# Optimization experiments

Measured on AMD Instinct MI355X. Metric: run time of the kernel, lower is better.

The kernel has to match this reference:

```python
import jax, jax.numpy as jnp
import numpy as np

B, T, D = 4, 4096, 768      # batch, tokens, n_embd
S = 1024                    # memory_slots (divides T -> adaptive pool == window mean)
K = 8                       # memory_topk
RW = 0.1                    # memory_retrieval_weight


def setup_inputs() -> dict:
    key = jax.random.key(0)
    ks = jax.random.split(key, 10)
    w = 1.0 / np.sqrt(D).astype(np.float32)
    return {
        "x": jax.random.normal(ks[0], (B, T, D), jnp.float32),
        "Wq": jax.random.normal(ks[1], (D, D), jnp.float32) * w,
        "bq": jnp.zeros((D,), jnp.float32),
        "Wk": jax.random.normal(ks[2], (D, D), jnp.float32) * w,
        "bk": jnp.zeros((D,), jnp.float32),
        "Wv": jax.random.normal(ks[3], (D, D), jnp.float32) * w,
        "bv": jnp.zeros((D,), jnp.float32),
        "Wp": jax.random.normal(ks[4], (D, D), jnp.float32) * w,
        "bp": jnp.zeros((D,), jnp.float32),
        "persistent_memory": jax.random.normal(ks[5], (S, D), jnp.float32),
    }


def reference(x, Wq, bq, Wk, bk, Wv, bv, Wp, bp, persistent_memory):
    # _build_memory_slots: adaptive_avg_pool1d to S slots; T % S == 0 so it is a window mean
    pooled = x.reshape(B, S, T // S, D).mean(axis=2)                    # [B,S,D]
    pers = jnp.broadcast_to(persistent_memory[None], (B, S, D))         # persistent bank
    slots = jnp.concatenate([pooled, pers], axis=1)                     # [B,2S,D]

    q = x @ Wq + bq                                                     # [B,T,D]
    k = slots @ Wk + bk                                                 # [B,2S,D]
    v = slots @ Wv + bv                                                 # [B,2S,D]

    scores = jnp.einsum('btd,bsd->bts', q, k) / jnp.sqrt(jnp.float32(D))  # [B,T,2S]
    top_s, top_i = jax.lax.top_k(scores, K)                             # [B,T,K]
    w = jax.nn.softmax(top_s, axis=-1)                                  # softmax over top-k only

    # gather top-k values: [B,T,K,D]
    vg = jnp.take_along_axis(v, top_i.reshape(B, T * K)[:, :, None], axis=1)
    vg = vg.reshape(B, T, K, D)
    retrieved = jnp.einsum('btk,btkd->btd', w, vg)                      # weighted combine

    return RW * (retrieved @ Wp + bp)                                   # proj * retrieval_weight
```

## Files before the change

kernel.cpp:

```cpp
#include <hip/hip_runtime.h>
#include <math.h>

#define BB 4
#define TT 4096
#define DD 768
#define SS 1024
#define S2 2048
#define KTOP 8
#define RWEIGHT 0.1f
#define TAU 2e-4f
#define AMB_CAP 256

typedef __attribute__((ext_vector_type(8))) _Float16 f16x8;
typedef __attribute__((ext_vector_type(4))) float f32x4;
typedef _Float16 f16;

__global__ __launch_bounds__(256) void build_pooled_all(
    const float* __restrict__ x, float* __restrict__ slots)
{
    int i = blockIdx.x * 256 + threadIdx.x;
    int s2 = i / DD;
    int d = i - s2 * DD;
    int b = s2 >> 10, s = s2 & 1023;
    const float* xb = x + (size_t)b * TT * DD + (size_t)(4 * s) * DD + d;
    slots[i] = 0.25f * (xb[0] + xb[DD] + xb[2 * DD] + xb[3 * DD]);
}

__global__ __launch_bounds__(256) void transpose_split(
    const float* __restrict__ W0, const float* __restrict__ W1,
    const float* __restrict__ W2, const float* __restrict__ W3,
    f16* __restrict__ WQh, f16* __restrict__ WQm,
    f16* __restrict__ WKh, f16* __restrict__ WKm,
    f16* __restrict__ WVh, f16* __restrict__ WPh,
    float* __restrict__ WkT32)
{
    const int z = blockIdx.z;
    const float* W = (z == 0) ? W0 : (z == 1) ? W1 : (z == 2) ? W2 : W3;
    __shared__ float t[32][33];
    int bx = blockIdx.x * 32, by = blockIdx.y * 32;
    int lx = threadIdx.x & 31, ly = threadIdx.x >> 5;
#pragma unroll
    for (int r = 0; r < 32; r += 8)
        t[ly + r][lx] = W[(size_t)(bx + ly + r) * 768 + by + lx];
    __syncthreads();
#pragma unroll
    for (int r = 0; r < 32; r += 8) {
        float w = t[lx][ly + r];
        size_t idx = (size_t)(by + ly + r) * 768 + bx + lx;
        f16 h = (f16)w;
        if (z == 0) { WQh[idx] = h; WQm[idx] = (f16)(w - (float)h); }
        else if (z == 1) { WKh[idx] = h; WKm[idx] = (f16)(w - (float)h); WkT32[idx] = w; }
        else if (z == 2) { WVh[idx] = h; }
        else { WPh[idx] = h; }
    }
}

__global__ void zeroN(int* p) { p[threadIdx.x] = 0; }

__device__ __forceinline__ void tile_split_prod(
    const float* __restrict__ A, int arow0,
    const f16* __restrict__ Bh, const f16* __restrict__ Bm, int bncol,
    const float* __restrict__ bias,
    f16* __restrict__ Ch, f16* __restrict__ Cm, int crow0,
    f16* LAh, f16* LAm, f16* LBh, f16* LBm)
{
    const int tid = threadIdx.x;
    const int lane = tid & 63;
    const int wc = (tid >> 6) & 1;
    const int wr = (tid >> 7) & 1;
    const int srow = tid >> 1, c0 = tid & 1;
    const int p0 = c0 ^ (srow & 3) ^ ((srow >> 2) & 1);
    const int wo0 = srow * 32 + p0 * 8, wo1 = wo0 ^ 16;
    const int csw = (((lane >> 4) ^ (lane & 3) ^ ((lane >> 2) & 1)) * 8);
    const size_t bn = (size_t)bncol;

    f32x4 acc[4][4];
#pragma unroll
    for (int i = 0; i < 4; ++i)
#pragma unroll
        for (int j = 0; j < 4; ++j) acc[i][j] = (f32x4){0.f, 0.f, 0.f, 0.f};

    const float* pa = A + (size_t)(arow0 + srow) * 768 + c0 * 8;
    const f16* pbh = Bh + (bn + srow) * 768 + c0 * 8;
    const f16* pbm = Bm + (bn + srow) * 768 + c0 * 8;

    for (int k0 = 0; k0 < 768; k0 += 32) {
        float4 a0 = *(const float4*)(pa + k0);
        float4 a1 = *(const float4*)(pa + k0 + 4);
        float4 a2 = *(const float4*)(pa + k0 + 16);
        float4 a3 = *(const float4*)(pa + k0 + 20);
        f16x8 bh0 = *(const f16x8*)(pbh + k0);
        f16x8 bh1 = *(const f16x8*)(pbh + k0 + 16);
        f16x8 bm0 = *(const f16x8*)(pbm + k0);
        f16x8 bm1 = *(const f16x8*)(pbm + k0 + 16);
        __syncthreads();
        {
            float av[16] = {a0.x, a0.y, a0.z, a0.w, a1.x, a1.y, a1.z, a1.w,
                            a2.x, a2.y, a2.z, a2.w, a3.x, a3.y, a3.z, a3.w};
            f16x8 h, m;
#pragma unroll
            for (int j = 0; j < 8; ++j) {
                f16 hh = (f16)av[j]; h[j] = hh; m[j] = (f16)(av[j] - (float)hh);
            }
            *(f16x8*)&LAh[wo0] = h; *(f16x8*)&LAm[wo0] = m;
#pragma unroll
            for (int j = 0; j < 8; ++j) {
                f16 hh = (f16)av[j + 8]; h[j] = hh; m[j] = (f16)(av[j + 8] - (float)hh);
            }
            *(f16x8*)&LAh[wo1] = h; *(f16x8*)&LAm[wo1] = m;
            *(f16x8*)&LBh[wo0] = bh0; *(f16x8*)&LBh[wo1] = bh1;
            *(f16x8*)&LBm[wo0] = bm0; *(f16x8*)&LBm[wo1] = bm1;
        }
        __syncthreads();

        f16x8 fah[4], fam[4], fbh[4], fbm[4];
#pragma unroll
        for (int mi = 0; mi < 4; ++mi) {
            int off = (wr * 64 + mi * 16 + (lane & 15)) * 32 + csw;
            fah[mi] = *(const f16x8*)&LAh[off];
            fam[mi] = *(const f16x8*)&LAm[off];
        }
#pragma unroll
        for (int ni = 0; ni < 4; ++ni) {
            int off = (wc * 64 + ni * 16 + (lane & 15)) * 32 + csw;
            fbh[ni] = *(const f16x8*)&LBh[off];
            fbm[ni] = *(const f16x8*)&LBm[off];
        }
#pragma unroll
        for (int mi = 0; mi < 4; ++mi)
#pragma unroll
            for (int ni = 0; ni < 4; ++ni) {
                acc[mi][ni] = __builtin_amdgcn_mfma_f32_16x16x32_f16(
                    fah[mi], fbh[ni], acc[mi][ni], 0, 0, 0);
                acc[mi][ni] = __builtin_amdgcn_mfma_f32_16x16x32_f16(
                    fah[mi], fbm[ni], acc[mi][ni], 0, 0, 0);
                acc[mi][ni] = __builtin_amdgcn_mfma_f32_16x16x32_f16(
                    fam[mi], fbh[ni], acc[mi][ni], 0, 0, 0);
            }
    }

    const int orow0 = wr * 64 + (lane >> 4) * 4;
    const int ocol0 = wc * 64 + (lane & 15);
#pragma unroll
    for (int mi = 0; mi < 4; ++mi)
#pragma unroll
        for (int ni = 0; ni < 4; ++ni) {
            size_t col = bn + ocol0 + ni * 16;
            float badd = bias[col];
            size_t rbase = (size_t)crow0 + orow0 + mi * 16;
#pragma unroll
            for (int r = 0; r < 4; ++r) {
                float val = acc[mi][ni][r] + badd;
                f16 h = (f16)val;
                size_t idx = (rbase + r) * 768 + col;
                Ch[idx] = h;
                Cm[idx] = (f16)(val - (float)h);
            }
        }
}

__device__ __forceinline__ void tile_1p_prod(
    const float* __restrict__ A, int arow0,
    const f16* __restrict__ Bh, int bncol,
    const float* __restrict__ bias,
    f16* __restrict__ Co, int crow0, f16* LA, f16* LB)
{
    const int tid = threadIdx.x;
    const int lane = tid & 63;
    const int wc = (tid >> 6) & 1;
    const int wr = (tid >> 7) & 1;
    const int srow = tid >> 1, c0 = tid & 1;
    const int p0 = c0 ^ (srow & 3) ^ ((srow >> 2) & 1);
    const int wo0 = srow * 32 + p0 * 8, wo1 = wo0 ^ 16;
    const int csw = (((lane >> 4) ^ (lane & 3) ^ ((lane >> 2) & 1)) * 8);
    const size_t bn = (size_t)bncol;

    f32x4 acc[4][4];
#pragma unroll
    for (int i = 0; i < 4; ++i)
#pragma unroll
        for (int j = 0; j < 4; ++j) acc[i][j] = (f32x4){0.f, 0.f, 0.f, 0.f};

    const float* pa = A + (size_t)(arow0 + srow) * 768 + c0 * 8;
    const f16* pbh = Bh + (bn + srow) * 768 + c0 * 8;

    for (int k0 = 0; k0 < 768; k0 += 32) {
        float4 a0 = *(const float4*)(pa + k0);
        float4 a1 = *(const float4*)(pa + k0 + 4);
        float4 a2 = *(const float4*)(pa + k0 + 16);
        float4 a3 = *(const float4*)(pa + k0 + 20);
        f16x8 bh0 = *(const f16x8*)(pbh + k0);
        f16x8 bh1 = *(const f16x8*)(pbh + k0 + 16);
        __syncthreads();
        {
            f16x8 h;
            h[0] = (f16)a0.x; h[1] = (f16)a0.y; h[2] = (f16)a0.z; h[3] = (f16)a0.w;
            h[4] = (f16)a1.x; h[5] = (f16)a1.y; h[6] = (f16)a1.z; h[7] = (f16)a1.w;
            *(f16x8*)&LA[wo0] = h;
            h[0] = (f16)a2.x; h[1] = (f16)a2.y; h[2] = (f16)a2.z; h[3] = (f16)a2.w;
            h[4] = (f16)a3.x; h[5] = (f16)a3.y; h[6] = (f16)a3.z; h[7] = (f16)a3.w;
            *(f16x8*)&LA[wo1] = h;
            *(f16x8*)&LB[wo0] = bh0;
            *(f16x8*)&LB[wo1] = bh1;
        }
        __syncthreads();
        f16x8 fah[4], fbh[4];
#pragma unroll
        for (int mi = 0; mi < 4; ++mi)
            fah[mi] = *(const f16x8*)&LA[(wr * 64 + mi * 16 + (lane & 15)) * 32 + csw];
#pragma unroll
        for (int ni = 0; ni < 4; ++ni)
            fbh[ni] = *(const f16x8*)&LB[(wc * 64 + ni * 16 + (lane & 15)) * 32 + csw];
#pragma unroll
        for (int mi = 0; mi < 4; ++mi)
#pragma unroll
            for (int ni = 0; ni < 4; ++ni)
                acc[mi][ni] = __builtin_amdgcn_mfma_f32_16x16x32_f16(
                    fah[mi], fbh[ni], acc[mi][ni], 0, 0, 0);
    }

    const int orow0 = wr * 64 + (lane >> 4) * 4;
    const int ocol0 = wc * 64 + (lane & 15);
#pragma unroll
    for (int mi = 0; mi < 4; ++mi)
#pragma unroll
        for (int ni = 0; ni < 4; ++ni) {
            size_t col = bn + ocol0 + ni * 16;
            float badd = bias[col];
            size_t rbase = (size_t)crow0 + orow0 + mi * 16;
#pragma unroll
            for (int r = 0; r < 4; ++r)
                Co[(rbase + r) * 768 + col] = (f16)(acc[mi][ni][r] + badd);
        }
}

__device__ __forceinline__ void tile_proj(
    const f16* __restrict__ A, int arow0,
    const f16* __restrict__ Bh, int bncol,
    const float* __restrict__ bias,
    float* __restrict__ Co, int crow0, f16* LA, f16* LB)
{
    const int tid = threadIdx.x;
    const int lane = tid & 63;
    const int wc = (tid >> 6) & 1;
    const int wr = (tid >> 7) & 1;
    const int srow = tid >> 1, c0 = tid & 1;
    const int p0 = c0 ^ (srow & 3) ^ ((srow >> 2) & 1);
    const int wo0 = srow * 32 + p0 * 8, wo1 = wo0 ^ 16;
    const int csw = (((lane >> 4) ^ (lane & 3) ^ ((lane >> 2) & 1)) * 8);
    const size_t bn = (size_t)bncol;

    f32x4 acc[4][4];
#pragma unroll
    for (int i = 0; i < 4; ++i)
#pragma unroll
        for (int j = 0; j < 4; ++j) acc[i][j] = (f32x4){0.f, 0.f, 0.f, 0.f};

    const f16* pa = A + (size_t)(arow0 + srow) * 768 + c0 * 8;
    const f16* pbh = Bh + (bn + srow) * 768 + c0 * 8;

    for (int k0 = 0; k0 < 768; k0 += 32) {
        f16x8 ah0 = *(const f16x8*)(pa + k0);
        f16x8 ah1 = *(const f16x8*)(pa + k0 + 16);
        f16x8 bh0 = *(const f16x8*)(pbh + k0);
        f16x8 bh1 = *(const f16x8*)(pbh + k0 + 16);
        __syncthreads();
        *(f16x8*)&LA[wo0] = ah0; *(f16x8*)&LA[wo1] = ah1;
        *(f16x8*)&LB[wo0] = bh0; *(f16x8*)&LB[wo1] = bh1;
        __syncthreads();
        f16x8 fah[4], fbh[4];
#pragma unroll
        for (int mi = 0; mi < 4; ++mi)
            fah[mi] = *(const f16x8*)&LA[(wr * 64 + mi * 16 + (lane & 15)) * 32 + csw];
#pragma unroll
        for (int ni = 0; ni < 4; ++ni)
            fbh[ni] = *(const f16x8*)&LB[(wc * 64 + ni * 16 + (lane & 15)) * 32 + csw];
#pragma unroll
        for (int mi = 0; mi < 4; ++mi)
#pragma unroll
            for (int ni = 0; ni < 4; ++ni)
                acc[mi][ni] = __builtin_amdgcn_mfma_f32_16x16x32_f16(
                    fah[mi], fbh[ni], acc[mi][ni], 0, 0, 0);
    }

    const int orow0 = wr * 64 + (lane >> 4) * 4;
    const int ocol0 = wc * 64 + (lane & 15);
#pragma unroll
    for (int mi = 0; mi < 4; ++mi)
#pragma unroll
        for (int ni = 0; ni < 4; ++ni) {
            size_t col = bn + ocol0 + ni * 16;
            float badd = RWEIGHT * bias[col];
            size_t rbase = (size_t)crow0 + orow0 + mi * 16;
#pragma unroll
            for (int r = 0; r < 4; ++r)
                Co[(rbase + r) * 768 + col] = RWEIGHT * acc[mi][ni][r] + badd;
        }
}

__device__ __forceinline__ void tile_scores_planes(
    const f16* __restrict__ qh, const f16* __restrict__ qm, int arow0,
    const f16* __restrict__ kh, const f16* __restrict__ km, int bncol,
    float* __restrict__ C, float alpha,
    f16* LAh, f16* LAm, f16* LBh, f16* LBm)
{
    const int tid = threadIdx.x;
    const int lane = tid & 63;
    const int wc = (tid >> 6) & 1;
    const int wr = (tid >> 7) & 1;
    const int srow = tid >> 1, c0 = tid & 1;
    const int p0 = c0 ^ (srow & 3) ^ ((srow >> 2) & 1);
    const int wo0 = srow * 32 + p0 * 8, wo1 = wo0 ^ 16;
    const int csw = (((lane >> 4) ^ (lane & 3) ^ ((lane >> 2) & 1)) * 8);
    const size_t bn = (size_t)bncol;

    f32x4 acc[4][4];
#pragma unroll
    for (int i = 0; i < 4; ++i)
#pragma unroll
        for (int j = 0; j < 4; ++j) acc[i][j] = (f32x4){0.f, 0.f, 0.f, 0.f};

    const f16* pah = qh + (size_t)(arow0 + srow) * 768 + c0 * 8;
    const f16* pam = qm + (size_t)(arow0 + srow) * 768 + c0 * 8;
    const f16* pbh = kh + (bn + srow) * 768 + c0 * 8;
    const f16* pbm = km + (bn + srow) * 768 + c0 * 8;

    for (int k0 = 0; k0 < 768; k0 += 32) {
        f16x8 ah0 = *(const f16x8*)(pah + k0);
        f16x8 ah1 = *(const f16x8*)(pah + k0 + 16);
        f16x8 am0 = *(const f16x8*)(pam + k0);
        f16x8 am1 = *(const f16x8*)(pam + k0 + 16);
        f16x8 bh0 = *(const f16x8*)(pbh + k0);
        f16x8 bh1 = *(const f16x8*)(pbh + k0 + 16);
        f16x8 bm0 = *(const f16x8*)(pbm + k0);
        f16x8 bm1 = *(const f16x8*)(pbm + k0 + 16);
        __syncthreads();
        *(f16x8*)&LAh[wo0] = ah0; *(f16x8*)&LAh[wo1] = ah1;
        *(f16x8*)&LAm[wo0] = am0; *(f16x8*)&LAm[wo1] = am1;
        *(f16x8*)&LBh[wo0] = bh0; *(f16x8*)&LBh[wo1] = bh1;
        *(f16x8*)&LBm[wo0] = bm0; *(f16x8*)&LBm[wo1] = bm1;
        __syncthreads();

        f16x8 fah[4], fam[4], fbh[4], fbm[4];
#pragma unroll
        for (int mi = 0; mi < 4; ++mi) {
            int off = (wr * 64 + mi * 16 + (lane & 15)) * 32 + csw;
            fah[mi] = *(const f16x8*)&LAh[off];
            fam[mi] = *(const f16x8*)&LAm[off];
        }
#pragma unroll
        for (int ni = 0; ni < 4; ++ni) {
            int off = (wc * 64 + ni * 16 + (lane & 15)) * 32 + csw;
            fbh[ni] = *(const f16x8*)&LBh[off];
            fbm[ni] = *(const f16x8*)&LBm[off];
        }
#pragma unroll
        for (int mi = 0; mi < 4; ++mi)
#pragma unroll
            for (int ni = 0; ni < 4; ++ni) {
                acc[mi][ni] = __builtin_amdgcn_mfma_f32_16x16x32_f16(
                    fah[mi], fbh[ni], acc[mi][ni], 0, 0, 0);
                acc[mi][ni] = __builtin_amdgcn_mfma_f32_16x16x32_f16(
                    fah[mi], fbm[ni], acc[mi][ni], 0, 0, 0);
                acc[mi][ni] = __builtin_amdgcn_mfma_f32_16x16x32_f16(
                    fam[mi], fbh[ni], acc[mi][ni], 0, 0, 0);
            }
    }

    const int orow0 = wr * 64 + (lane >> 4) * 4;
    const int ocol0 = wc * 64 + (lane & 15);
#pragma unroll
    for (int mi = 0; mi < 4; ++mi)
#pragma unroll
        for (int ni = 0; ni < 4; ++ni) {
            size_t col = bn + ocol0 + ni * 16;
            size_t rbase = (size_t)arow0 + orow0 + mi * 16;
#pragma unroll
            for (int r = 0; r < 4; ++r)
                C[(rbase + r) * S2 + col] = alpha * acc[mi][ni][r];
        }
}

__global__ __launch_bounds__(256) void megaSelProd(
    int nSel, const float* __restrict__ scores, const f16* __restrict__ v16r,
    f16* __restrict__ retrW, int gbase,
    int* __restrict__ ambc, int* __restrict__ ambgrow, int* __restrict__ cand,
    float* __restrict__ oldw, f16* __restrict__ vsave,
    int hasQ, int hasKV, int doPm,
    const float* __restrict__ xq, const float* __restrict__ slots_b,
    const float* __restrict__ pm,
    const f16* __restrict__ WQh, const f16* __restrict__ WQm,
    const f16* __restrict__ WKh, const f16* __restrict__ WKm,
    const f16* __restrict__ WVh,
    const float* __restrict__ bq, const float* __restrict__ bk,
    const float* __restrict__ bv,
    f16* __restrict__ qh, f16* __restrict__ qm,
    f16* __restrict__ kh, f16* __restrict__ km,
    f16* __restrict__ v16w, f16* __restrict__ v16w2)
{
    __shared__ f16 LAh[4096], LAm[4096], LBh[4096], LBm[4096];
    int t = blockIdx.x;

    if (hasQ) {
        if (t < 192) {
            tile_split_prod(xq, (t / 6) * 128, WQh, WQm, (t % 6) * 128, bq,
                            qh, qm, (t / 6) * 128, LAh, LAm, LBh, LBm);
            return;
        }
        t -= 192;
    }
    if (hasKV) {
        if (t < 48) {
            tile_split_prod(slots_b, (t / 6) * 128, WKh, WKm, (t % 6) * 128, bk,
                            kh, km, (t / 6) * 128, LAh, LAm, LBh, LBm);
            return;
        }
        t -= 48;
        if (doPm) {
            if (t < 48) {
                tile_split_prod(pm, (t / 6) * 128, WKh, WKm, (t % 6) * 128, bk,
                                kh, km, 1024 + (t / 6) * 128, LAh, LAm, LBh, LBm);
                return;
            }
            t -= 48;
        }
        if (t < 48) {
            tile_1p_prod(slots_b, (t / 6) * 128, WVh, (t % 6) * 128, bv,
                         v16w, (t / 6) * 128, LAh, LBh);
            return;
        }
        t -= 48;
        if (doPm) {
            if (t < 48) {
                tile_1p_prod(pm, (t / 6) * 128, WVh, (t % 6) * 128, bv,
                             v16w, 1024 + (t / 6) * 128, LAh, LBh);
                return;
            }
            t -= 48;
            if (t < 48) {
                tile_1p_prod(pm, (t / 6) * 128, WVh, (t % 6) * 128, bv,
                             v16w2, 1024 + (t / 6) * 128, LAh, LBh);
                return;
            }
            t -= 48;
        }
    }
    if (t >= nSel) return;

    const int lane = threadIdx.x & 63;
    const int wave = threadIdx.x >> 6;
    const int row = t * 4 + wave;
    const float* srow = scores + (size_t)row * S2;
    float vals[32];
#pragma unroll
    for (int i = 0; i < 32; ++i) vals[i] = srow[lane + (i << 6)];

    float topv[16]; int topi[16];
    bool amb = false;
    int nr = 9;
    for (int r = 0; r < 16; ++r) {
        if (r >= nr) break;
        float bvv = -3.4e38f; int bii = 0x7fffffff;
#pragma unroll
        for (int i = 0; i < 32; ++i)
            if (vals[i] > bvv) { bvv = vals[i]; bii = lane + (i << 6); }
#pragma unroll
        for (int off = 32; off > 0; off >>= 1) {
            float ov = __shfl_xor(bvv, off);
            int   oi = __shfl_xor(bii, off);
            if (ov > bvv || (ov == bvv && oi < bii)) { bvv = ov; bii = oi; }
        }
        topv[r] = bvv; topi[r] = bii;
        if ((bii & 63) == lane) vals[bii >> 6] = -3.4e38f;
        if (r == 8) {
            amb = (topv[7] - topv[8]) < TAU;
            if (amb) nr = 16;
        }
    }

    float m = topv[0], w[KTOP], sum = 0.f;
#pragma unroll
    for (int r = 0; r < KTOP; ++r) { w[r] = expf(topv[r] - m); sum += w[r]; }
    float inv = 1.f / sum;
#pragma unroll
    for (int r = 0; r < KTOP; ++r) w[r] *= inv;

    if (amb) {
        int idx = 0;
        if (lane == 0) idx = atomicAdd(ambc, 1);
        idx = __shfl(idx, 0);
        if (idx < AMB_CAP) {
            if (lane == 0) ambgrow[idx] = gbase + row;
            if (lane < 16) cand[idx * 16 + lane] = topi[lane];
            if (lane < KTOP) oldw[idx * KTOP + lane] = w[lane];
            f16* vs = vsave + (size_t)idx * 16 * 768;
            for (int cc = lane; cc < 16 * 96; cc += 64) {
                int cr = cc / 96, ch = cc - cr * 96;
                *(f16x8*)&vs[(size_t)cr * 768 + ch * 8] =
                    *(const f16x8*)&v16r[(size_t)topi[cr] * 768 + ch * 8];
            }
        }
    }

    for (int c = lane; c < 96; c += 64) {
        float o[8] = {0, 0, 0, 0, 0, 0, 0, 0};
#pragma unroll
        for (int r = 0; r < KTOP; ++r) {
            f16x8 vv = *(const f16x8*)&v16r[(size_t)topi[r] * 768 + c * 8];
#pragma unroll
            for (int j = 0; j < 8; ++j) o[j] += w[r] * (float)vv[j];
        }
        f16x8 hx;
#pragma unroll
        for (int j = 0; j < 8; ++j) hx[j] = (f16)o[j];
        *(f16x8*)&retrW[(size_t)row * 768 + c * 8] = hx;
    }
}

__global__ __launch_bounds__(256) void megaScoresProj(
    int nSc, const f16* __restrict__ qh, const f16* __restrict__ qm,
    const f16* __restrict__ kh, const f16* __restrict__ km,
    float* __restrict__ scores, float alpha,
    const f16* __restrict__ retrR, const f16* __restrict__ WPh,
    const float* __restrict__ bp, float* __restrict__ outp)
{
    __shared__ f16 LAh[4096], LAm[4096], LBh[4096], LBm[4096];
    int t = blockIdx.x;
    if (t < nSc) {
        tile_scores_planes(qh, qm, (t >> 4) * 128, kh, km, (t & 15) * 128,
                           scores, alpha, LAh, LAm, LBh, LBm);
        return;
    }
    t -= nSc;
    tile_proj(retrR, (t / 6) * 128, WPh, (t % 6) * 128, bp,
              outp, (t / 6) * 128, LAh, LBh);
}

__global__ __launch_bounds__(256) void fixA(
    const int* __restrict__ amb_count, const int* __restrict__ amb_grow,
    const float* __restrict__ x, const float* __restrict__ Wq,
    const float* __restrict__ bq, double* __restrict__ q64buf)
{
    int n = *amb_count; if (n > AMB_CAP) n = AMB_CAP;
    const int i = blockIdx.y;
    if (i >= n) return;
    const int tid = threadIdx.x;
    const int jl = tid & 63;
    const int ks = tid >> 6;
    const int j = blockIdx.x * 64 + jl;
    const int grow = amb_grow[i];

    __shared__ float xs[768];
    __shared__ double ps[4][64];
    for (int t = tid; t < 768; t += 256) xs[t] = x[(size_t)grow * 768 + t];
    __syncthreads();

    double a0 = 0.0, a1 = 0.0;
    const float* wp = Wq + j;
    const int k0 = ks * 192;
#pragma unroll 8
    for (int k = 0; k < 192; k += 2) {
        a0 = fma((double)xs[k0 + k],     (double)wp[(size_t)(k0 + k) * 768],     a0);
        a1 = fma((double)xs[k0 + k + 1], (double)wp[(size_t)(k0 + k + 1) * 768], a1);
    }
    ps[ks][jl] = a0 + a1;
    __syncthreads();
    if (ks == 0)
        q64buf[(size_t)i * 768 + j] =
            ((ps[0][jl] + ps[1][jl]) + (ps[2][jl] + ps[3][jl])) + (double)bq[j];
}

__global__ __launch_bounds__(256) void fixB(
    const int* __restrict__ amb_count,
    const float* __restrict__ WkT, const float* __restrict__ bk,
    const double* __restrict__ q64buf,
    double* __restrict__ ubuf, double* __restrict__ bkqbuf)
{
    int n = *amb_count; if (n > AMB_CAP) n = AMB_CAP;
    const int i = blockIdx.y;
    if (i >= n) return;
    const int tid = threadIdx.x;
    const int tl = tid & 63;
    const int js = tid >> 6;
    const int t = blockIdx.x * 64 + tl;

    __shared__ double qs[768];
    __shared__ double ps[4][64];
    const double* qrow = q64buf + (size_t)i * 768;
    for (int k = tid; k < 768; k += 256) qs[k] = qrow[k];
    __syncthreads();

    double a0 = 0.0, a1 = 0.0;
    const float* wp = WkT + t;
    const int j0 = js * 192;
#pragma unroll 8
    for (int k = 0; k < 192; k += 2) {
        a0 = fma((double)wp[(size_t)(j0 + k) * 768],     qs[j0 + k],     a0);
        a1 = fma((double)wp[(size_t)(j0 + k + 1) * 768], qs[j0 + k + 1], a1);
    }
    ps[js][tl] = a0 + a1;
    __syncthreads();
    if (js == 0)
        ubuf[(size_t)i * 768 + t] = (ps[0][tl] + ps[1][tl]) + (ps[2][tl] + ps[3][tl]);

    if (blockIdx.x == 0 && tid < 64) {
        double p = 0.0;
#pragma unroll
        for (int c = 0; c < 12; ++c) {
            int jj = tid + (c << 6);
            p = fma((double)bk[jj], qs[jj], p);
        }
#pragma unroll
        for (int off = 32; off; off >>= 1) p += __shfl_xor(p, off);
        if (tid == 0) bkqbuf[i] = p;
    }
}

__global__ __launch_bounds__(256) void fixC(
    const int* __restrict__ amb_count, const int* __restrict__ amb_grow,
    const float* __restrict__ x, const float* __restrict__ pm,
    const int* __restrict__ cand, const float* __restrict__ oldw,
    const double* __restrict__ ubuf, const double* __restrict__ bkqbuf,
    const f16* __restrict__ vsave, float* __restrict__ dret)
{
    int n = *amb_count; if (n > AMB_CAP) n = AMB_CAP;
    const int i = blockIdx.x;
    if (i >= n) return;
    const int tid = threadIdx.x;
    const int lane = tid & 63;
    const int wave = tid >> 6;
    const int grow = amb_grow[i];
    const float* xb = x + (size_t)(grow >> 12) * TT * 768;

    __shared__ double us[768];
    __shared__ double cs_s[16];
    __shared__ float coef[16];

    const double* urow = ubuf + (size_t)i * 768;
    for (int t = tid; t < 768; t += 256) us[t] = urow[t];
    __syncthreads();

    const double ISQ = 1.0 / sqrt((double)DD);
    const double bkq = bkqbuf[i];
#pragma unroll
    for (int c = wave; c < 16; c += 4) {
        int s = cand[i * 16 + c];
        double p = 0.0;
        if (s < SS) {
            const float* xr = xb + (size_t)(4 * s) * 768;
#pragma unroll
            for (int t = 0; t < 12; ++t) {
                int j2 = lane + (t << 6);
                double sv = 0.25 * ((double)xr[j2] + (double)xr[j2 + 768] +
                                    (double)xr[j2 + 1536] + (double)xr[j2 + 2304]);
                p = fma(sv, us[j2], p);
            }
        } else {
            const float* pr = pm + (size_t)(s - SS) * 768;
#pragma unroll
            for (int t = 0; t < 12; ++t) {
                int j2 = lane + (t << 6);
                p = fma((double)pr[j2], us[j2], p);
            }
        }
#pragma unroll
        for (int off = 32; off; off >>= 1) p += __shfl_xor(p, off);
        if (lane == 0) cs_s[c] = (p + bkq) * ISQ;
    }
    __syncthreads();

    if (tid == 0) {
        double cs[16]; int ci[16];
        for (int c = 0; c < 16; ++c) { cs[c] = cs_s[c]; ci[c] = cand[i * 16 + c]; }
        unsigned used = 0;
        double sv[KTOP]; int sp[KTOP];
        for (int r = 0; r < KTOP; ++r) {
            int bi = -1;
            for (int c = 0; c < 16; ++c) {
                if (used & (1u << c)) continue;
                if (bi < 0 || cs[c] > cs[bi] ||
                    (cs[c] == cs[bi] && ci[c] < ci[bi])) bi = c;
            }
            used |= (1u << bi); sv[r] = cs[bi]; sp[r] = bi;
        }
        double mx = sv[0], es[KTOP], ssum = 0.0;
        for (int r = 0; r < KTOP; ++r) { es[r] = exp(sv[r] - mx); ssum += es[r]; }
        for (int c = 0; c < 16; ++c) coef[c] = (c < KTOP) ? -oldw[i * KTOP + c] : 0.f;
        for (int r = 0; r < KTOP; ++r) coef[sp[r]] += (float)(es[r] / ssum);
    }
    __syncthreads();

    const f16* vs = vsave + (size_t)i * 16 * 768;
    for (int j = tid; j < 768; j += 256) {
        float d = 0.f;
#pragma unroll
        for (int c = 0; c < 16; ++c) d += coef[c] * (float)vs[(size_t)c * 768 + j];
        dret[(size_t)i * 768 + j] = d;
    }
}

__global__ __launch_bounds__(256) void fixD(
    const int* __restrict__ amb_count, const int* __restrict__ amb_grow,
    const float* __restrict__ dret, const float* __restrict__ Wp,
    float* __restrict__ out)
{
    int n = *amb_count; if (n > AMB_CAP) n = AMB_CAP;
    const int i = blockIdx.y;
    if (i >= n) return;
    const int tid = threadIdx.x;
    const int jl = tid & 63;
    const int ks = tid >> 6;
    const int j = blockIdx.x * 64 + jl;
    const int grow = amb_grow[i];

    __shared__ float ds[768];
    __shared__ float ps[4][64];
    for (int t = tid; t < 768; t += 256) ds[t] = dret[(size_t)i * 768 + t];
    __syncthreads();

    float a0 = 0.f, a1 = 0.f;
    const float* wp = Wp + j;
    const int k0 = ks * 192;
#pragma unroll 8
    for (int k = 0; k < 192; k += 2) {
        a0 = fmaf(ds[k0 + k],     wp[(size_t)(k0 + k) * 768],     a0);
        a1 = fmaf(ds[k0 + k + 1], wp[(size_t)(k0 + k + 1) * 768], a1);
    }
    ps[ks][jl] = a0 + a1;
    __syncthreads();
    if (ks == 0)
        out[(size_t)grow * 768 + j] +=
            RWEIGHT * ((ps[0][jl] + ps[1][jl]) + (ps[2][jl] + ps[3][jl]));
}

extern "C" void kernel_launch(void* const* d_in, const int* in_sizes, int n_in,
                              void* d_out, int out_size, void* d_ws, size_t ws_size,
                              hipStream_t stream)
{
    const float* x  = (const float*)d_in[0];
    const float* Wq = (const float*)d_in[1];
    const float* bq = (const float*)d_in[2];
    const float* Wk = (const float*)d_in[3];
    const float* bk = (const float*)d_in[4];
    const float* Wv = (const float*)d_in[5];
    const float* bv = (const float*)d_in[6];
    const float* Wp = (const float*)d_in[7];
    const float* bp = (const float*)d_in[8];
    const float* pm = (const float*)d_in[9];
    float* out = (float*)d_out;
    float* ws  = (float*)d_ws;

    const float inv_sqrt_d = (float)(1.0 / sqrt((double)DD));
    const size_t TD  = (size_t)TT * DD;
    const size_t SD  = (size_t)SS * DD;
    const size_t WSZ = (size_t)DD * DD;

    float* p = ws;
    f16* WQh = (f16*)p; p += WSZ / 2;
    f16* WQm = (f16*)p; p += WSZ / 2;
    f16* WKh = (f16*)p; p += WSZ / 2;
    f16* WKm = (f16*)p; p += WSZ / 2;
    f16* WVh = (f16*)p; p += WSZ / 2;
    f16* WPh = (f16*)p; p += WSZ / 2;
    float* WkT32 = p; p += WSZ;
    float* slots_all = p; p += (size_t)BB * SD;
    f16* qh = (f16*)p; p += TD / 2;
    f16* qm = (f16*)p; p += TD / 2;
    f16* kh = (f16*)p; p += SD;
    f16* km = (f16*)p; p += SD;
    f16* v16a = (f16*)p; p += SD;
    f16* v16b = (f16*)p; p += SD;
    f16* retrA = (f16*)p; p += TD / 2;
    f16* retrB = (f16*)p; p += TD / 2;
    double* q64buf = (double*)p; p += (size_t)AMB_CAP * DD * 2;
    double* ubuf   = (double*)p; p += (size_t)AMB_CAP * DD * 2;
    double* bkqbuf = (double*)p; p += AMB_CAP * 2;
    int* cand = (int*)p; p += (size_t)AMB_CAP * 16;
    float* oldw = p; p += (size_t)AMB_CAP * KTOP;
    f16* vsave = (f16*)p; p += (size_t)AMB_CAP * 16 * DD / 2;
    float* dret = p; p += (size_t)AMB_CAP * DD;
    int* ambc = (int*)p; p += 64;
    int* ambgrow = (int*)p; p += AMB_CAP;
    float* scores = p;

    transpose_split<<<dim3(24, 24, 4), 256, 0, stream>>>(
        Wq, Wk, Wv, Wp, WQh, WQm, WKh, WKm, WVh, WPh, WkT32);
    zeroN<<<1, 64, 0, stream>>>(ambc);
    build_pooled_all<<<(BB * SS * DD) / 256, 256, 0, stream>>>(x, slots_all);

    megaSelProd<<<432, 256, 0, stream>>>(
        0, nullptr, nullptr, nullptr, 0, ambc, ambgrow, cand, oldw, vsave,
        1, 1, 1, x, slots_all, pm,
        WQh, WQm, WKh, WKm, WVh, bq, bk, bv, qh, qm, kh, km, v16a, v16b);
    megaScoresProj<<<512, 256, 0, stream>>>(
        512, qh, qm, kh, km, scores, inv_sqrt_d, nullptr, WPh, bp, nullptr);

    for (int b = 1; b < BB; ++b) {
        f16* v16w = (b & 1) ? v16b : v16a;
        f16* v16r = ((b - 1) & 1) ? v16b : v16a;
        f16* retrW = ((b - 1) & 1) ? retrB : retrA;

        megaSelProd<<<1312, 256, 0, stream>>>(
            1024, scores, v16r, retrW, (b - 1) * TT,
            ambc, ambgrow, cand, oldw, vsave,
            1, 1, 0, x + (size_t)b * TD, slots_all + (size_t)b * SD, nullptr,
            WQh, WQm, WKh, WKm, WVh, bq, bk, bv, qh, qm, kh, km, v16w, nullptr);
        megaScoresProj<<<704, 256, 0, stream>>>(
            512, qh, qm, kh, km, scores, inv_sqrt_d,
            retrW, WPh, bp, out + (size_t)(b - 1) * TD);
    }

    f16* v16r3 = v16b;
    f16* retrW3 = retrB;
    megaSelProd<<<1024, 256, 0, stream>>>(
        1024, scores, v16r3, retrW3, 3 * TT,
        ambc, ambgrow, cand, oldw, vsave,
        0, 0, 0, nullptr, nullptr, nullptr,
        WQh, WQm, WKh, WKm, WVh, bq, bk, bv, qh, qm, kh, km, nullptr, nullptr);
    megaScoresProj<<<192, 256, 0, stream>>>(
        0, nullptr, nullptr, nullptr, nullptr, nullptr, 0.f,
        retrW3, WPh, bp, out + (size_t)3 * TD);

    fixA<<<dim3(12, AMB_CAP), 256, 0, stream>>>(ambc, ambgrow, x, Wq, bq, q64buf);
    fixB<<<dim3(12, AMB_CAP), 256, 0, stream>>>(ambc, WkT32, bk, q64buf, ubuf, bkqbuf);
    fixC<<<AMB_CAP, 256, 0, stream>>>(ambc, ambgrow, x, pm, cand, oldw,
                                      ubuf, bkqbuf, vsave, dret);
    fixD<<<dim3(12, AMB_CAP), 256, 0, stream>>>(ambc, ambgrow, dret, Wp, out);
}
```

Measured before the change: 643.1 us.

## Store f16 operands in MFMA fragment-packed layout and load fragments directly from global

Weights, Q/K planes and the retrieved activations are written in a layout packed into 16x32 MFMA fragments. The GEMM tiles then load B (and both operands for scores and projection) straight from global memory with coalesced per-lane loads, skipping the LDS staging and its barriers. A-operand global loads in the projection tiles are software-pipelined one k-step ahead. In exchange, operands are re-read from global/L2 by each wave with no LDS sharing between waves, which may raise cache traffic. Any consumer that still expects row-major q/k/retr buffers would read the wrong data.

```diff
diff --git a/kernel.cpp b/kernel.cpp
--- a/kernel.cpp
+++ b/kernel.cpp
@@ -15,6 +15,11 @@
 typedef __attribute__((ext_vector_type(4))) float f32x4;
 typedef _Float16 f16;
 
+__device__ __forceinline__ size_t fragoff(int row, int k) {
+    return ((size_t)(row >> 4) * 24 + (k >> 5)) * 512 +
+           (((row & 15) + (((k >> 3) & 3) << 4)) << 3) + (k & 7);
+}
+
 __global__ __launch_bounds__(256) void build_pooled_all(
     const float* __restrict__ x, float* __restrict__ slots)
 {
@@ -46,12 +51,14 @@
 #pragma unroll
     for (int r = 0; r < 32; r += 8) {
         float w = t[lx][ly + r];
-        size_t idx = (size_t)(by + ly + r) * 768 + bx + lx;
+        int n = by + ly + r, k = bx + lx;
+        size_t fo = fragoff(n, k);
         f16 h = (f16)w;
-        if (z == 0) { WQh[idx] = h; WQm[idx] = (f16)(w - (float)h); }
-        else if (z == 1) { WKh[idx] = h; WKm[idx] = (f16)(w - (float)h); WkT32[idx] = w; }
-        else if (z == 2) { WVh[idx] = h; }
-        else { WPh[idx] = h; }
+        if (z == 0) { WQh[fo] = h; WQm[fo] = (f16)(w - (float)h); }
+        else if (z == 1) { WKh[fo] = h; WKm[fo] = (f16)(w - (float)h);
+                           WkT32[(size_t)n * 768 + k] = w; }
+        else if (z == 2) { WVh[fo] = h; }
+        else { WPh[fo] = h; }
     }
 }
 
@@ -59,10 +66,10 @@
 
 __device__ __forceinline__ void tile_split_prod(
     const float* __restrict__ A, int arow0,
-    const f16* __restrict__ Bh, const f16* __restrict__ Bm, int bncol,
+    const f16* __restrict__ BhF, const f16* __restrict__ BmF, int bncol,
     const float* __restrict__ bias,
-    f16* __restrict__ Ch, f16* __restrict__ Cm, int crow0,
-    f16* LAh, f16* LAm, f16* LBh, f16* LBm)
+    f16* __restrict__ ChF, f16* __restrict__ CmF, int crow0,
+    f16* LAh, f16* LAm)
 {
     const int tid = threadIdx.x;
     const int lane = tid & 63;
@@ -72,7 +79,6 @@
     const int p0 = c0 ^ (srow & 3) ^ ((srow >> 2) & 1);
     const int wo0 = srow * 32 + p0 * 8, wo1 = wo0 ^ 16;
     const int csw = (((lane >> 4) ^ (lane & 3) ^ ((lane >> 2) & 1)) * 8);
-    const size_t bn = (size_t)bncol;
 
     f32x4 acc[4][4];
 #pragma unroll
@@ -81,18 +87,14 @@
         for (int j = 0; j < 4; ++j) acc[i][j] = (f32x4){0.f, 0.f, 0.f, 0.f};
 
     const float* pa = A + (size_t)(arow0 + srow) * 768 + c0 * 8;
-    const f16* pbh = Bh + (bn + srow) * 768 + c0 * 8;
-    const f16* pbm = Bm + (bn + srow) * 768 + c0 * 8;
-
-    for (int k0 = 0; k0 < 768; k0 += 32) {
-        float4 a0 = *(const float4*)(pa + k0);
-        float4 a1 = *(const float4*)(pa + k0 + 4);
-        float4 a2 = *(const float4*)(pa + k0 + 16);
-        float4 a3 = *(const float4*)(pa + k0 + 20);
-        f16x8 bh0 = *(const f16x8*)(pbh + k0);
-        f16x8 bh1 = *(const f16x8*)(pbh + k0 + 16);
-        f16x8 bm0 = *(const f16x8*)(pbm + k0);
-        f16x8 bm1 = *(const f16x8*)(pbm + k0 + 16);
+    const int rbB0 = bncol / 16 + wc * 4;
+
+    float4 a0 = *(const float4*)(pa);
+    float4 a1 = *(const float4*)(pa + 4);
+    float4 a2 = *(const float4*)(pa + 16);
+    float4 a3 = *(const float4*)(pa + 20);
+
+    for (int kb = 0; kb < 24; ++kb) {
         __syncthreads();
         {
             float av[16] = {a0.x, a0.y, a0.z, a0.w, a1.x, a1.y, a1.z, a1.w,
@@ -108,23 +110,30 @@
                 f16 hh = (f16)av[j + 8]; h[j] = hh; m[j] = (f16)(av[j + 8] - (float)hh);
             }
             *(f16x8*)&LAh[wo1] = h; *(f16x8*)&LAm[wo1] = m;
-            *(f16x8*)&LBh[wo0] = bh0; *(f16x8*)&LBh[wo1] = bh1;
-            *(f16x8*)&LBm[wo0] = bm0; *(f16x8*)&LBm[wo1] = bm1;
         }
         __syncthreads();
 
-        f16x8 fah[4], fam[4], fbh[4], fbm[4];
+        if (kb + 1 < 24) {
+            int k0 = (kb + 1) * 32;
+            a0 = *(const float4*)(pa + k0);
+            a1 = *(const float4*)(pa + k0 + 4);
+            a2 = *(const float4*)(pa + k0 + 16);
+            a3 = *(const float4*)(pa + k0 + 20);
+        }
+
+        f16x8 fbh[4], fbm[4];
+#pragma unroll
+        for (int ni = 0; ni < 4; ++ni) {
+            size_t off = ((size_t)(rbB0 + ni) * 24 + kb) * 512 + lane * 8;
+            fbh[ni] = *(const f16x8*)&BhF[off];
+            fbm[ni] = *(const f16x8*)&BmF[off];
+        }
+        f16x8 fah[4], fam[4];
 #pragma unroll
         for (int mi = 0; mi < 4; ++mi) {
             int off = (wr * 64 + mi * 16 + (lane & 15)) * 32 + csw;
             fah[mi] = *(const f16x8*)&LAh[off];
             fam[mi] = *(const f16x8*)&LAm[off];
-        }
-#pragma unroll
-        for (int ni = 0; ni < 4; ++ni) {
-            int off = (wc * 64 + ni * 16 + (lane & 15)) * 32 + csw;
-            fbh[ni] = *(const f16x8*)&LBh[off];
-            fbm[ni] = *(const f16x8*)&LBm[off];
         }
 #pragma unroll
         for (int mi = 0; mi < 4; ++mi)
@@ -145,25 +154,25 @@
     for (int mi = 0; mi < 4; ++mi)
 #pragma unroll
         for (int ni = 0; ni < 4; ++ni) {
-            size_t col = bn + ocol0 + ni * 16;
-            float badd = bias[col];
-            size_t rbase = (size_t)crow0 + orow0 + mi * 16;
+            int kk = bncol + ocol0 + ni * 16;
+            float badd = bias[kk];
+            int rbase = crow0 + orow0 + mi * 16;
 #pragma unroll
             for (int r = 0; r < 4; ++r) {
                 float val = acc[mi][ni][r] + badd;
                 f16 h = (f16)val;
-                size_t idx = (rbase + r) * 768 + col;
-                Ch[idx] = h;
-                Cm[idx] = (f16)(val - (float)h);
+                size_t fo = fragoff(rbase + r, kk);
+                ChF[fo] = h;
+                CmF[fo] = (f16)(val - (float)h);
             }
         }
 }
 
 __device__ __forceinline__ void tile_1p_prod(
     const float* __restrict__ A, int arow0,
-    const f16* __restrict__ Bh, int bncol,
+    const f16* __restrict__ BhF, int bncol,
     const float* __restrict__ bias,
-    f16* __restrict__ Co, int crow0, f16* LA, f16* LB)
+    f16* __restrict__ Co, int crow0, f16* LA)
 {
     const int tid = threadIdx.x;
     const int lane = tid & 63;
@@ -173,7 +182,6 @@
     const int p0 = c0 ^ (srow & 3) ^ ((srow >> 2) & 1);
     const int wo0 = srow * 32 + p0 * 8, wo1 = wo0 ^ 16;
     const int csw = (((lane >> 4) ^ (lane & 3) ^ ((lane >> 2) & 1)) * 8);
-    const size_t bn = (size_t)bncol;
 
     f32x4 acc[4][4];
 #pragma unroll
@@ -182,15 +190,14 @@
         for (int j = 0; j < 4; ++j) acc[i][j] = (f32x4){0.f, 0.f, 0.f, 0.f};
 
     const float* pa = A + (size_t)(arow0 + srow) * 768 + c0 * 8;
-    const f16* pbh = Bh + (bn + srow) * 768 + c0 * 8;
-
-    for (int k0 = 0; k0 < 768; k0 += 32) {
-        float4 a0 = *(const float4*)(pa + k0);
-        float4 a1 = *(const float4*)(pa + k0 + 4);
-        float4 a2 = *(const float4*)(pa + k0 + 16);
-        float4 a3 = *(const float4*)(pa + k0 + 20);
-        f16x8 bh0 = *(const f16x8*)(pbh + k0);
-        f16x8 bh1 = *(const f16x8*)(pbh + k0 + 16);
+    const int rbB0 = bncol / 16 + wc * 4;
+
+    float4 a0 = *(const float4*)(pa);
+    float4 a1 = *(const float4*)(pa + 4);
+    float4 a2 = *(const float4*)(pa + 16);
+    float4 a3 = *(const float4*)(pa + 20);
+
+    for (int kb = 0; kb < 24; ++kb) {
         __syncthreads();
         {
             f16x8 h;
@@ -200,17 +207,25 @@
             h[0] = (f16)a2.x; h[1] = (f16)a2.y; h[2] = (f16)a2.z; h[3] = (f16)a2.w;
             h[4] = (f16)a3.x; h[5] = (f16)a3.y; h[6] = (f16)a3.z; h[7] = (f16)a3.w;
             *(f16x8*)&LA[wo1] = h;
-            *(f16x8*)&LB[wo0] = bh0;
-            *(f16x8*)&LB[wo1] = bh1;
         }
         __syncthreads();
-        f16x8 fah[4], fbh[4];
+
+        if (kb + 1 < 24) {
+            int k0 = (kb + 1) * 32;
+            a0 = *(const float4*)(pa + k0);
+            a1 = *(const float4*)(pa + k0 + 4);
+            a2 = *(const float4*)(pa + k0 + 16);
+            a3 = *(const float4*)(pa + k0 + 20);
+        }
+
+        f16x8 fbh[4];
+#pragma unroll
+        for (int ni = 0; ni < 4; ++ni)
+            fbh[ni] = *(const f16x8*)&BhF[((size_t)(rbB0 + ni) * 24 + kb) * 512 + lane * 8];
+        f16x8 fah[4];
 #pragma unroll
         for (int mi = 0; mi < 4; ++mi)
             fah[mi] = *(const f16x8*)&LA[(wr * 64 + mi * 16 + (lane & 15)) * 32 + csw];
-#pragma unroll
-        for (int ni = 0; ni < 4; ++ni)
-            fbh[ni] = *(const f16x8*)&LB[(wc * 64 + ni * 16 + (lane & 15)) * 32 + csw];
 #pragma unroll
         for (int mi = 0; mi < 4; ++mi)
 #pragma unroll
@@ -225,7 +240,7 @@
     for (int mi = 0; mi < 4; ++mi)
 #pragma unroll
         for (int ni = 0; ni < 4; ++ni) {
-            size_t col = bn + ocol0 + ni * 16;
+            size_t col = (size_t)bncol + ocol0 + ni * 16;
             float badd = bias[col];
             size_t rbase = (size_t)crow0 + orow0 + mi * 16;
 #pragma unroll
@@ -234,21 +249,16 @@
         }
 }
 
-__device__ __forceinline__ void tile_proj(
-    const f16* __restrict__ A, int arow0,
-    const f16* __restrict__ Bh, int bncol,
+__device__ __forceinline__ void tile_proj_frag(
+    const f16* __restrict__ AF, int arow0,
+    const f16* __restrict__ BhF, int bncol,
     const float* __restrict__ bias,
-    float* __restrict__ Co, int crow0, f16* LA, f16* LB)
+    float* __restrict__ Co, int crow0)
 {
     const int tid = threadIdx.x;
     const int lane = tid & 63;
     const int wc = (tid >> 6) & 1;
     const int wr = (tid >> 7) & 1;
-    const int srow = tid >> 1, c0 = tid & 1;
-    const int p0 = c0 ^ (srow & 3) ^ ((srow >> 2) & 1);
-    const int wo0 = srow * 32 + p0 * 8, wo1 = wo0 ^ 16;
-    const int csw = (((lane >> 4) ^ (lane & 3) ^ ((lane >> 2) & 1)) * 8);
-    const size_t bn = (size_t)bncol;
 
     f32x4 acc[4][4];
 #pragma unroll
@@ -256,25 +266,17 @@
 #pragma unroll
         for (int j = 0; j < 4; ++j) acc[i][j] = (f32x4){0.f, 0.f, 0.f, 0.f};
 
-    const f16* pa = A + (size_t)(arow0 + srow) * 768 + c0 * 8;
-    const f16* pbh = Bh + (bn + srow) * 768 + c0 * 8;
-
-    for (int k0 = 0; k0 < 768; k0 += 32) {
-        f16x8 ah0 = *(const f16x8*)(pa + k0);
-        f16x8 ah1 = *(const f16x8*)(pa + k0 + 16);
-        f16x8 bh0 = *(const f16x8*)(pbh + k0);
-        f16x8 bh1 = *(const f16x8*)(pbh + k0 + 16);
-        __syncthreads();
-        *(f16x8*)&LA[wo0] = ah0; *(f16x8*)&LA[wo1] = ah1;
-        *(f16x8*)&LB[wo0] = bh0; *(f16x8*)&LB[wo1] = bh1;
-        __syncthreads();
+    const int rbA0 = arow0 / 16 + wr * 4;
+    const int rbB0 = bncol / 16 + wc * 4;
+
+    for (int kb = 0; kb < 24; ++kb) {
         f16x8 fah[4], fbh[4];
 #pragma unroll
         for (int mi = 0; mi < 4; ++mi)
-            fah[mi] = *(const f16x8*)&LA[(wr * 64 + mi * 16 + (lane & 15)) * 32 + csw];
+            fah[mi] = *(const f16x8*)&AF[((size_t)(rbA0 + mi) * 24 + kb) * 512 + lane * 8];
 #pragma unroll
         for (int ni = 0; ni < 4; ++ni)
-            fbh[ni] = *(const f16x8*)&LB[(wc * 64 + ni * 16 + (lane & 15)) * 32 + csw];
+            fbh[ni] = *(const f16x8*)&BhF[((size_t)(rbB0 + ni) * 24 + kb) * 512 + lane * 8];
 #pragma unroll
         for (int mi = 0; mi < 4; ++mi)
 #pragma unroll
@@ -289,7 +291,7 @@
     for (int mi = 0; mi < 4; ++mi)
 #pragma unroll
         for (int ni = 0; ni < 4; ++ni) {
-            size_t col = bn + ocol0 + ni * 16;
+            size_t col = (size_t)bncol + ocol0 + ni * 16;
             float badd = RWEIGHT * bias[col];
             size_t rbase = (size_t)crow0 + orow0 + mi * 16;
 #pragma unroll
@@ -298,21 +300,15 @@
         }
 }
 
-__device__ __forceinline__ void tile_scores_planes(
-    const f16* __restrict__ qh, const f16* __restrict__ qm, int arow0,
-    const f16* __restrict__ kh, const f16* __restrict__ km, int bncol,
-    float* __restrict__ C, float alpha,
-    f16* LAh, f16* LAm, f16* LBh, f16* LBm)
+__device__ __forceinline__ void tile_scores_frag(
+    const f16* __restrict__ qhF, const f16* __restrict__ qmF, int arow0,
+    const f16* __restrict__ khF, const f16* __restrict__ kmF, int bncol,
+    float* __restrict__ C, float alpha)
 {
     const int tid = threadIdx.x;
     const int lane = tid & 63;
     const int wc = (tid >> 6) & 1;
     const int wr = (tid >> 7) & 1;
-    const int srow = tid >> 1, c0 = tid & 1;
-    const int p0 = c0 ^ (srow & 3) ^ ((srow >> 2) & 1);
-    const int wo0 = srow * 32 + p0 * 8, wo1 = wo0 ^ 16;
-    const int csw = (((lane >> 4) ^ (lane & 3) ^ ((lane >> 2) & 1)) * 8);
-    const size_t bn = (size_t)bncol;
 
     f32x4 acc[4][4];
 #pragma unroll
@@ -320,39 +316,22 @@
 #pragma unroll
         for (int j = 0; j < 4; ++j) acc[i][j] = (f32x4){0.f, 0.f, 0.f, 0.f};
 
-    const f16* pah = qh + (size_t)(arow0 + srow) * 768 + c0 * 8;
-    const f16* pam = qm + (size_t)(arow0 + srow) * 768 + c0 * 8;
-    const f16* pbh = kh + (bn + srow) * 768 + c0 * 8;
-    const f16* pbm = km + (bn + srow) * 768 + c0 * 8;
-
-    for (int k0 = 0; k0 < 768; k0 += 32) {
-        f16x8 ah0 = *(const f16x8*)(pah + k0);
-        f16x8 ah1 = *(const f16x8*)(pah + k0 + 16);
-        f16x8 am0 = *(const f16x8*)(pam + k0);
-        f16x8 am1 = *(const f16x8*)(pam + k0 + 16);
-        f16x8 bh0 = *(const f16x8*)(pbh + k0);
-        f16x8 bh1 = *(const f16x8*)(pbh + k0 + 16);
-        f16x8 bm0 = *(const f16x8*)(pbm + k0);
-        f16x8 bm1 = *(const f16x8*)(pbm + k0 + 16);
-        __syncthreads();
-        *(f16x8*)&LAh[wo0] = ah0; *(f16x8*)&LAh[wo1] = ah1;
-        *(f16x8*)&LAm[wo0] = am0; *(f16x8*)&LAm[wo1] = am1;
-        *(f16x8*)&LBh[wo0] = bh0; *(f16x8*)&LBh[wo1] = bh1;
-        *(f16x8*)&LBm[wo0] = bm0; *(f16x8*)&LBm[wo1] = bm1;
-        __syncthreads();
-
+    const int rbA0 = arow0 / 16 + wr * 4;
+    const int rbB0 = bncol / 16 + wc * 4;
+
+    for (int kb = 0; kb < 24; ++kb) {
         f16x8 fah[4], fam[4], fbh[4], fbm[4];
 #pragma unroll
         for (int mi = 0; mi < 4; ++mi) {
-            int off = (wr * 64 + mi * 16 + (lane & 15)) * 32 + csw;
-            fah[mi] = *(const f16x8*)&LAh[off];
-            fam[mi] = *(const f16x8*)&LAm[off];
+            size_t off = ((size_t)(rbA0 + mi) * 24 + kb) * 512 + lane * 8;
+            fah[mi] = *(const f16x8*)&qhF[off];
+            fam[mi] = *(const f16x8*)&qmF[off];
         }
 #pragma unroll
         for (int ni = 0; ni < 4; ++ni) {
-            int off = (wc * 64 + ni * 16 + (lane & 15)) * 32 + csw;
-            fbh[ni] = *(const f16x8*)&LBh[off];
-            fbm[ni] = *(const f16x8*)&LBm[off];
+            size_t off = ((size_t)(rbB0 + ni) * 24 + kb) * 512 + lane * 8;
+            fbh[ni] = *(const f16x8*)&khF[off];
+            fbm[ni] = *(const f16x8*)&kmF[off];
         }
 #pragma unroll
         for (int mi = 0; mi < 4; ++mi)
@@ -373,7 +352,7 @@
     for (int mi = 0; mi < 4; ++mi)
 #pragma unroll
         for (int ni = 0; ni < 4; ++ni) {
-            size_t col = bn + ocol0 + ni * 16;
+            size_t col = (size_t)bncol + ocol0 + ni * 16;
             size_t rbase = (size_t)arow0 + orow0 + mi * 16;
 #pragma unroll
             for (int r = 0; r < 4; ++r)
@@ -398,13 +377,13 @@
     f16* __restrict__ kh, f16* __restrict__ km,
     f16* __restrict__ v16w, f16* __restrict__ v16w2)
 {
-    __shared__ f16 LAh[4096], LAm[4096], LBh[4096], LBm[4096];
+    __shared__ f16 LAh[4096], LAm[4096];
     int t = blockIdx.x;
 
     if (hasQ) {
         if (t < 192) {
             tile_split_prod(xq, (t / 6) * 128, WQh, WQm, (t % 6) * 128, bq,
-                            qh, qm, (t / 6) * 128, LAh, LAm, LBh, LBm);
+                            qh, qm, (t / 6) * 128, LAh, LAm);
             return;
         }
         t -= 192;
@@ -412,34 +391,34 @@
     if (hasKV) {
         if (t < 48) {
             tile_split_prod(slots_b, (t / 6) * 128, WKh, WKm, (t % 6) * 128, bk,
-                            kh, km, (t / 6) * 128, LAh, LAm, LBh, LBm);
+                            kh, km, (t / 6) * 128, LAh, LAm);
             return;
         }
         t -= 48;
         if (doPm) {
             if (t < 48) {
                 tile_split_prod(pm, (t / 6) * 128, WKh, WKm, (t % 6) * 128, bk,
-                                kh, km, 1024 + (t / 6) * 128, LAh, LAm, LBh, LBm);
+                                kh, km, 1024 + (t / 6) * 128, LAh, LAm);
                 return;
             }
             t -= 48;
         }
         if (t < 48) {
             tile_1p_prod(slots_b, (t / 6) * 128, WVh, (t % 6) * 128, bv,
-                         v16w, (t / 6) * 128, LAh, LBh);
+                         v16w, (t / 6) * 128, LAh);
             return;
         }
         t -= 48;
         if (doPm) {
             if (t < 48) {
                 tile_1p_prod(pm, (t / 6) * 128, WVh, (t % 6) * 128, bv,
-                             v16w, 1024 + (t / 6) * 128, LAh, LBh);
+                             v16w, 1024 + (t / 6) * 128, LAh);
                 return;
             }
             t -= 48;
             if (t < 48) {
                 tile_1p_prod(pm, (t / 6) * 128, WVh, (t % 6) * 128, bv,
-                             v16w2, 1024 + (t / 6) * 128, LAh, LBh);
+                             v16w2, 1024 + (t / 6) * 128, LAh);
                 return;
             }
             t -= 48;
@@ -513,7 +492,9 @@
         f16x8 hx;
 #pragma unroll
         for (int j = 0; j < 8; ++j) hx[j] = (f16)o[j];
-        *(f16x8*)&retrW[(size_t)row * 768 + c * 8] = hx;
+        size_t fo = ((size_t)(row >> 4) * 24 + (c >> 2)) * 512 +
+                    (((row & 15) + ((c & 3) << 4)) << 3);
+        *(f16x8*)&retrW[fo] = hx;
     }
 }
 
@@ -524,16 +505,15 @@
     const f16* __restrict__ retrR, const f16* __restrict__ WPh,
     const float* __restrict__ bp, float* __restrict__ outp)
 {
-    __shared__ f16 LAh[4096], LAm[4096], LBh[4096], LBm[4096];
     int t = blockIdx.x;
     if (t < nSc) {
-        tile_scores_planes(qh, qm, (t >> 4) * 128, kh, km, (t & 15) * 128,
-                           scores, alpha, LAh, LAm, LBh, LBm);
+        tile_scores_frag(qh, qm, (t >> 4) * 128, kh, km, (t & 15) * 128,
+                         scores, alpha);
         return;
     }
     t -= nSc;
-    tile_proj(retrR, (t / 6) * 128, WPh, (t % 6) * 128, bp,
-              outp, (t / 6) * 128, LAh, LBh);
+    tile_proj_frag(retrR, (t / 6) * 128, WPh, (t % 6) * 128, bp,
+                   outp, (t / 6) * 128);
 }
 
 __global__ __launch_bounds__(256) void fixA(
```

New measurement: 663.9 us. 3.2% more time.
